# Kernel optimization log

Measured on AMD Instinct MI355X. Metric: run time of the kernel, lower is better.

## Reference

```python
import jax, jax.numpy as jnp
import numpy as np

B, L, C, H, FF = 2, 2048, 1024, 16, 4096
HD = C // H
SCALE = HD ** -0.5
EPS = 1e-5


def _ln(x, g, b):
    m = jnp.mean(x, axis=-1, keepdims=True)
    v = jnp.mean((x - m) ** 2, axis=-1, keepdims=True)
    return (x - m) * jax.lax.rsqrt(v + EPS) * g + b


def setup_inputs() -> dict:
    key = jax.random.key(0)
    ks = jax.random.split(key, 12)
    s = lambda fan_in: 1.0 / np.sqrt(fan_in)
    return {
        "x": jax.random.normal(ks[0], (B, L, C), jnp.float32),
        "freq_diff": jax.random.normal(ks[1], (B, L), jnp.float32),
        "qkv_w": jax.random.normal(ks[2], (C, 3 * C), jnp.float32) * s(C),
        "qkv_b": jnp.zeros((3 * C,), jnp.float32),
        "fp_w1": jax.random.normal(ks[3], (1, C), jnp.float32),
        "fp_b1": jnp.zeros((C,), jnp.float32),
        "fp_ln_g": jnp.ones((C,), jnp.float32),
        "fp_ln_b": jnp.zeros((C,), jnp.float32),
        "fp_w2": jax.random.normal(ks[4], (C, C), jnp.float32) * s(C),
        "fp_b2": jnp.zeros((C,), jnp.float32),
        "wq_w": jax.random.normal(ks[5], (HD, HD), jnp.float32) * s(HD),
        "wq_b": jnp.zeros((HD,), jnp.float32),
        "wk_w": jax.random.normal(ks[6], (HD, HD), jnp.float32) * s(HD),
        "wk_b": jnp.zeros((HD,), jnp.float32),
        "out_w": jax.random.normal(ks[7], (C, C), jnp.float32) * s(C),
        "out_b": jnp.zeros((C,), jnp.float32),
        "n1_g": jnp.ones((C,), jnp.float32),
        "n1_b": jnp.zeros((C,), jnp.float32),
        "n2_g": jnp.ones((C,), jnp.float32),
        "n2_b": jnp.zeros((C,), jnp.float32),
        "mlp_w1": jax.random.normal(ks[8], (C, FF), jnp.float32) * s(C),
        "mlp_b1": jnp.zeros((FF,), jnp.float32),
        "mlp_w2": jax.random.normal(ks[9], (FF, C), jnp.float32) * s(FF),
        "mlp_b2": jnp.zeros((C,), jnp.float32),
        "freq_scale": jnp.ones((1,), jnp.float32),
    }


def reference(x, freq_diff, qkv_w, qkv_b, fp_w1, fp_b1, fp_ln_g, fp_ln_b,
              fp_w2, fp_b2, wq_w, wq_b, wk_w, wk_b, out_w, out_b,
              n1_g, n1_b, n2_g, n2_b, mlp_w1, mlp_b1, mlp_w2, mlp_b2,
              freq_scale):
    shortcut = x
    xn = _ln(x, n1_g, n1_b)
    qkv = (xn @ qkv_w + qkv_b).reshape(B, L, 3, H, HD)
    qkv = jnp.transpose(qkv, (2, 0, 3, 1, 4))  # [3,B,H,L,HD]
    q, k, v = qkv[0], qkv[1], qkv[2]

    # frequency bias: MLP on scalar freq_diff -> per-head bias vectors
    fb = freq_diff[..., None] @ fp_w1 + fp_b1          # [B,L,C]
    fb = jax.nn.gelu(_ln(fb, fp_ln_g, fp_ln_b), approximate=False)
    fb = fb @ fp_w2 + fp_b2                            # [B,L,C]
    fb = jnp.transpose(fb.reshape(B, L, H, HD), (0, 2, 1, 3))  # [B,H,L,HD]
    qb = fb @ wq_w + wq_b
    kb = fb @ wk_w + wk_b
    freq_attn_bias = jnp.einsum('bhqd,bhkd->bhqk', qb, kb)

    attn = jnp.einsum('bhqd,bhkd->bhqk', q, k) * SCALE
    attn = attn + freq_scale[0] * freq_attn_bias
    attn = jax.nn.softmax(attn, axis=-1)
    o = jnp.einsum('bhqk,bhkd->bhqd', attn, v)
    o = jnp.transpose(o, (0, 2, 1, 3)).reshape(B, L, C)
    x = shortcut + (o @ out_w + out_b)

    xn2 = _ln(x, n2_g, n2_b)
    h = jax.nn.gelu(xn2 @ mlp_w1 + mlp_b1, approximate=False)
    x = x + (h @ mlp_w2 + mlp_b2)
    return x
```

## Files before the change

kernel.cpp:

```cpp
#include <hip/hip_runtime.h>
#include <math.h>


typedef __bf16 bf16;
typedef float f32x4 __attribute__((ext_vector_type(4)));
typedef bf16 bf16x8 __attribute__((ext_vector_type(8)));
typedef bf16 bf16x4 __attribute__((ext_vector_type(4)));

#define DEVINL __device__ __forceinline__

#define LOG2E 1.4426950408889634f

DEVINL float fast_exp2(float x) { return __builtin_amdgcn_exp2f(x); }

DEVINL void async_load16(const void* g, void* l) {
  __builtin_amdgcn_global_load_lds(
      (const __attribute__((address_space(1))) unsigned int*)g,
      (__attribute__((address_space(3))) unsigned int*)l, 16, 0, 0);
}

DEVINL f32x4 mfma16(bf16x8 a, bf16x8 b, f32x4 c) {
  return __builtin_amdgcn_mfma_f32_16x16x32_bf16(a, b, c, 0, 0, 0);
}

DEVINL float gelu_exact(float v) {
  return 0.5f * v * (1.0f + erff(v * 0.70710678118654752f));
}

DEVINL void hard_barrier() {
  asm volatile("" ::: "memory");
  __builtin_amdgcn_s_barrier();
  asm volatile("" ::: "memory");
}

DEVINL void block_reduce2(float& a, float& b, float* red, int tid) {
#pragma unroll
  for (int off = 32; off >= 1; off >>= 1) {
    a += __shfl_xor(a, off);
    b += __shfl_xor(b, off);
  }
  int w = tid >> 6;
  if ((tid & 63) == 0) { red[2 * w] = a; red[2 * w + 1] = b; }
  __syncthreads();
  a = red[0] + red[2] + red[4] + red[6];
  b = red[1] + red[3] + red[5] + red[7];
  __syncthreads();
}

__global__ __launch_bounds__(256) void pre_kernel(
    const float* __restrict__ qkv_w, const float* __restrict__ out_w,
    const float* __restrict__ mlp_w1, const float* __restrict__ mlp_w2,
    bf16* __restrict__ qkv_wt, bf16* __restrict__ out_wt,
    bf16* __restrict__ w1t, bf16* __restrict__ w2t,
    const float* __restrict__ x, const float* __restrict__ fd,
    const float* __restrict__ g1, const float* __restrict__ b1,
    const float* __restrict__ fw1, const float* __restrict__ fb1,
    const float* __restrict__ flg, const float* __restrict__ flb,
    bf16* __restrict__ xn, bf16* __restrict__ gout) {
  __shared__ float tile[32][33];
  __shared__ float red[8];
  const int id = blockIdx.x, t = threadIdx.x;
  if (id < 12288) {
    const float* W; bf16* Wt; int K, N, bx, by;
    if (id < 3072) {
      W = qkv_w; Wt = qkv_wt; K = 1024; N = 3072; bx = id % 96; by = id / 96;
    } else if (id < 4096) {
      int i = id - 3072;
      W = out_w; Wt = out_wt; K = 1024; N = 1024; bx = i & 31; by = i >> 5;
    } else if (id < 8192) {
      int i = id - 4096;
      W = mlp_w1; Wt = w1t; K = 1024; N = 4096; bx = i & 127; by = i >> 7;
    } else {
      int i = id - 8192;
      W = mlp_w2; Wt = w2t; K = 4096; N = 1024; bx = i & 31; by = i >> 5;
    }
    int n0 = bx * 32, k0 = by * 32;
    int tx = t & 31, ty = t >> 5;
#pragma unroll
    for (int r = 0; r < 4; ++r)
      tile[ty + r * 8][tx] = W[(size_t)(k0 + ty + r * 8) * N + n0 + tx];
    __syncthreads();
#pragma unroll
    for (int r = 0; r < 4; ++r)
      Wt[(size_t)(n0 + ty + r * 8) * K + k0 + tx] = (bf16)tile[tx][ty + r * 8];
    return;
  }
  int tok = id - 12288;
  float4 xv = ((const float4*)(x + (size_t)tok * 1024))[t];
  float s = xv.x + xv.y + xv.z + xv.w;
  float ss = xv.x * xv.x + xv.y * xv.y + xv.z * xv.z + xv.w * xv.w;
  block_reduce2(s, ss, red, t);
  float mean = s * (1.0f / 1024.0f);
  float rsig = rsqrtf(ss * (1.0f / 1024.0f) - mean * mean + 1e-5f);
  float4 g4 = ((const float4*)g1)[t], b4 = ((const float4*)b1)[t];
  bf16x4 o;
  o[0] = (bf16)((xv.x - mean) * rsig * g4.x + b4.x);
  o[1] = (bf16)((xv.y - mean) * rsig * g4.y + b4.y);
  o[2] = (bf16)((xv.z - mean) * rsig * g4.z + b4.z);
  o[3] = (bf16)((xv.w - mean) * rsig * g4.w + b4.w);
  ((bf16x4*)xn)[(size_t)tok * 256 + t] = o;

  float dv = fd[tok];
  float4 w4 = ((const float4*)fw1)[t], c4 = ((const float4*)fb1)[t];
  float f0 = dv * w4.x + c4.x, f1 = dv * w4.y + c4.y;
  float f2 = dv * w4.z + c4.z, f3 = dv * w4.w + c4.w;
  s = f0 + f1 + f2 + f3;
  ss = f0 * f0 + f1 * f1 + f2 * f2 + f3 * f3;
  block_reduce2(s, ss, red, t);
  mean = s * (1.0f / 1024.0f);
  rsig = rsqrtf(ss * (1.0f / 1024.0f) - mean * mean + 1e-5f);
  float4 lg = ((const float4*)flg)[t], lb = ((const float4*)flb)[t];
  bf16x4 q;
  q[0] = (bf16)gelu_exact((f0 - mean) * rsig * lg.x + lb.x);
  q[1] = (bf16)gelu_exact((f1 - mean) * rsig * lg.y + lb.y);
  q[2] = (bf16)gelu_exact((f2 - mean) * rsig * lg.z + lb.z);
  q[3] = (bf16)gelu_exact((f3 - mean) * rsig * lg.w + lb.w);
  ((bf16x4*)gout)[(size_t)tok * 256 + t] = q;
}

__global__ __launch_bounds__(256) void prec_qk(
    const float* __restrict__ fp_w2, const float* __restrict__ fp_b2,
    const float* __restrict__ wq_w, const float* __restrict__ wq_b,
    const float* __restrict__ wk_w, const float* __restrict__ wk_b,
    bf16* __restrict__ wqk2t, float* __restrict__ bqk) {
  __shared__ float Wl[64 * 64];
  __shared__ float Al[64 * 128];
  const int id = blockIdx.x;
  const int sel = id >> 7, h = (id >> 3) & 15, ck = id & 7;
  const int t = threadIdx.x;
  const float* wsel = sel ? wk_w : wq_w;
#pragma unroll
  for (int i = 0; i < 4; ++i)
    ((float4*)Wl)[i * 256 + t] = ((const float4*)wsel)[i * 256 + t];
  const int c0 = ck * 128, off = h * 64;
#pragma unroll
  for (int it = 0; it < 8; ++it) {
    int idx = it * 256 + t;
    int rr = idx >> 4, c4 = idx & 15;
    float4 v = *(const float4*)(fp_w2 + (size_t)(c0 + rr) * 1024 + off + c4 * 4);
    float vv[4] = {v.x, v.y, v.z, v.w};
#pragma unroll
    for (int k = 0; k < 4; ++k) {
      int i2 = c4 * 4 + k;
      Al[i2 * 128 + (rr ^ (i2 & 31))] = vv[k];
    }
  }
  __syncthreads();
  const int cr = t & 127, jh = (t >> 7) * 32;
  float acc[32];
#pragma unroll
  for (int j = 0; j < 32; ++j) acc[j] = 0.f;
  for (int i = 0; i < 64; ++i) {
    float a = Al[i * 128 + (cr ^ (i & 31))];
    const float4* wrow = (const float4*)(Wl + i * 64 + jh);
#pragma unroll
    for (int j4 = 0; j4 < 8; ++j4) {
      float4 wv = wrow[j4];
      acc[j4 * 4 + 0] += a * wv.x;
      acc[j4 * 4 + 1] += a * wv.y;
      acc[j4 * 4 + 2] += a * wv.z;
      acc[j4 * 4 + 3] += a * wv.w;
    }
  }
  const int nbase = sel * 1024 + off + jh;
#pragma unroll
  for (int j = 0; j < 32; ++j)
    wqk2t[(size_t)(nbase + j) * 1024 + c0 + cr] = (bf16)acc[j];
  if (ck == 0 && t < 64) {
    float s = 0.f;
    for (int i = 0; i < 64; ++i) s += fp_b2[off + i] * Wl[i * 64 + t];
    bqk[sel * 1024 + off + t] = s + (sel ? wk_b[t] : wq_b[t]);
  }
}

__global__ __launch_bounds__(256) void reduce_oln(
    const float* __restrict__ part, const float* __restrict__ x,
    const float* __restrict__ outb, const float* __restrict__ b2,
    const float* __restrict__ g, const float* __restrict__ bb,
    float* __restrict__ out0, bf16* __restrict__ ln2) {
  __shared__ float red[8];
  int tok = blockIdx.x, t = threadIdx.x;
  size_t base = (size_t)tok * 256 + t;
  const size_t S = (size_t)4096 * 256;
  float4 p0 = ((const float4*)part)[base];
  float4 p1 = ((const float4*)part)[base + S];
  float4 xv = ((const float4*)x)[base];
  float4 ob = ((const float4*)outb)[t];
  float v0 = xv.x + p0.x + p1.x + ob.x;
  float v1 = xv.y + p0.y + p1.y + ob.y;
  float v2 = xv.z + p0.z + p1.z + ob.z;
  float v3 = xv.w + p0.w + p1.w + ob.w;
  float s = v0 + v1 + v2 + v3;
  float ss = v0 * v0 + v1 * v1 + v2 * v2 + v3 * v3;
  block_reduce2(s, ss, red, t);
  float mean = s * (1.0f / 1024.0f);
  float rsig = rsqrtf(ss * (1.0f / 1024.0f) - mean * mean + 1e-5f);
  float4 g4 = ((const float4*)g)[t], bb4 = ((const float4*)bb)[t];
  bf16x4 o;
  o[0] = (bf16)((v0 - mean) * rsig * g4.x + bb4.x);
  o[1] = (bf16)((v1 - mean) * rsig * g4.y + bb4.y);
  o[2] = (bf16)((v2 - mean) * rsig * g4.z + bb4.z);
  o[3] = (bf16)((v3 - mean) * rsig * g4.w + bb4.w);
  ((bf16x4*)ln2)[base] = o;
  float4 b24 = ((const float4*)b2)[t];
  float4 ov;
  ov.x = v0 + b24.x; ov.y = v1 + b24.y; ov.z = v2 + b24.z; ov.w = v3 + b24.w;
  ((float4*)out0)[base] = ov;
}

#define PHASE(MH, NH, LA, LB, STAGE_STMT, WAIT_STMT)                          \
  do {                                                                        \
    if (LA) {                                                                 \
      _Pragma("unroll") for (int ml = 0; ml < 4; ++ml) {                      \
        _Pragma("unroll") for (int ks = 0; ks < 2; ++ks) {                    \
          const int rr = ml * 16 + lm;                                        \
          const int cc = (((ks * 4 + quad) ^ (lm & 7)) << 3);                 \
          af[ml][ks] = *(const bf16x8*)&As[bsel][MH][wm][rr][cc];             \
        }                                                                     \
      }                                                                       \
    }                                                                         \
    if (LB) {                                                                 \
      _Pragma("unroll") for (int nl = 0; nl < 2; ++nl) {                      \
        _Pragma("unroll") for (int ks = 0; ks < 2; ++ks) {                    \
          const int rr = nl * 16 + lm;                                        \
          const int cc = (((ks * 4 + quad) ^ (lm & 7)) << 3);                 \
          bfr[nl][ks] = *(const bf16x8*)&Bs[bsel][NH][wn][rr][cc];            \
        }                                                                     \
      }                                                                       \
    }                                                                         \
    STAGE_STMT;                                                               \
    WAIT_STMT;                                                                \
    hard_barrier();                                                           \
    __builtin_amdgcn_s_setprio(1);                                            \
    _Pragma("unroll") for (int ks = 0; ks < 2; ++ks) {                        \
      _Pragma("unroll") for (int ml = 0; ml < 4; ++ml) {                      \
        _Pragma("unroll") for (int nl = 0; nl < 2; ++nl) {                    \
          acc[(MH)*4 + ml][(NH)*2 + nl] = mfma16(                             \
              af[ml][ks], bfr[nl][ks], acc[(MH)*4 + ml][(NH)*2 + nl]);        \
        }                                                                     \
      }                                                                       \
    }                                                                         \
    __builtin_amdgcn_s_setprio(0);                                            \
  } while (0)

template <class Epi>
__global__ __launch_bounds__(512, 2) void gemm256(
    const bf16* __restrict__ A, const bf16* __restrict__ Bt,
    int lda, int ldb, int K, int kstride, int nbx, int nblk, int rowoffz,
    Epi epi) {
  __shared__ __align__(16) bf16 As[2][2][2][64][64];
  __shared__ __align__(16) bf16 Bs[2][2][4][32][64];

  const int tid = threadIdx.x;
  const int lane = tid & 63, w = tid >> 6;
  const int quad = lane >> 4, lm = lane & 15;
  const int wm = w >> 2, wn = w & 3;

  const int kz = blockIdx.x / nblk;
  const int bid = blockIdx.x - kz * nblk;
  const int swz = (nblk & 7) ? bid : ((bid & 7) * (nblk >> 3) + (bid >> 3));
  const int tm = swz / nbx, tn = swz - tm * nbx;
  const int m0 = tm << 8, n0 = tn << 8;
  const int rowoff = kz * rowoffz;
  A += (size_t)kz * kstride;
  Bt += (size_t)kz * kstride;

  const bf16* Abase = A + (size_t)m0 * lda;
  const bf16* Bbase = Bt + (size_t)n0 * ldb;

  auto stageA = [&](int b, int mh, int kt) {
#pragma unroll
    for (int j = 0; j < 2; ++j) {
      const int q = (w * 2 + j) * 64 + lane;
      const int wm2 = q >> 9, rr = (q >> 3) & 63, c = q & 7;
      async_load16(Abase + (size_t)(wm2 * 128 + mh * 64 + rr) * lda +
                       (size_t)kt * 64 + ((c ^ (rr & 7)) << 3),
                   (char*)&As[b][mh][0][0][0] + (w * 2 + j) * 1024);
    }
  };
  auto stageB = [&](int b, int nh, int kt) {
#pragma unroll
    for (int j = 0; j < 2; ++j) {
      const int q = (w * 2 + j) * 64 + lane;
      const int wn4 = q >> 8, rr = (q >> 3) & 31, c = q & 7;
      async_load16(Bbase + (size_t)(wn4 * 64 + nh * 32 + rr) * ldb +
                       (size_t)kt * 64 + ((c ^ (rr & 7)) << 3),
                   (char*)&Bs[b][nh][0][0][0] + (w * 2 + j) * 1024);
    }
  };

  f32x4 acc[8][4];
#pragma unroll
  for (int i = 0; i < 8; ++i)
#pragma unroll
    for (int j = 0; j < 4; ++j) {
      acc[i][j][0] = 0.f; acc[i][j][1] = 0.f;
      acc[i][j][2] = 0.f; acc[i][j][3] = 0.f;
    }
  bf16x8 af[4][2], bfr[2][2];

  stageA(0, 0, 0);
  stageB(0, 1, 0);
  stageA(0, 1, 0);
  stageB(0, 0, 0);
  stageA(1, 0, 1);
  stageB(1, 1, 1);
  asm volatile("s_waitcnt vmcnt(4)" ::: "memory");
  hard_barrier();

  const int nt = K >> 6;
  int bsel = 0;
  for (int t = 0; t < nt; ++t, bsel ^= 1) {
    PHASE(0, 0, 1, 1, { if (t + 1 < nt) stageA(bsel ^ 1, 1, t + 1); }, {});
    PHASE(0, 1, 0, 1, { if (t + 1 < nt) stageB(bsel ^ 1, 0, t + 1); }, {});
    PHASE(1, 1, 1, 0, { if (t + 2 < nt) stageA(bsel, 0, t + 2); }, {});
    PHASE(1, 0, 0, 1, { if (t + 2 < nt) stageB(bsel, 1, t + 2); },
          {
            if (t + 2 < nt) {
              asm volatile("s_waitcnt vmcnt(4)" ::: "memory");
            } else if (t + 1 < nt) {
              asm volatile("s_waitcnt vmcnt(0)" ::: "memory");
            }
          });
  }

#pragma unroll
  for (int mi = 0; mi < 8; ++mi)
#pragma unroll
    for (int ni = 0; ni < 4; ++ni)
      epi(rowoff + m0 + wm * 128 + mi * 16 + quad * 4,
          n0 + wn * 64 + ni * 16 + lm, acc[mi][ni]);
}

__global__ __launch_bounds__(256) void reduce_mlp2(
    const float* __restrict__ part, float* __restrict__ out) {
  size_t i = (size_t)blockIdx.x * 256 + threadIdx.x;
  const float4* p = (const float4*)part;
  float4 o = ((const float4*)out)[i];
  const size_t S = (size_t)4096 * 256;
  float4 a = p[i], b = p[i + S], c = p[i + 2 * S], d = p[i + 3 * S];
  o.x += a.x + b.x + c.x + d.x;
  o.y += a.y + b.y + c.y + d.y;
  o.z += a.z + b.z + c.z + d.z;
  o.w += a.w + b.w + c.w + d.w;
  ((float4*)out)[i] = o;
}

struct EpiQKV {
  const float* __restrict__ bias;
  bf16 *Qc, *Kc, *Vt;
  DEVINL void operator()(int row, int col, f32x4 v) const {
    int b = row >> 11, l = row & 2047;
    float bia = bias[col];
    if (col < 1024) {
      int h = col >> 6, d = col & 63;
      bf16* p = Qc + (size_t)(((b << 4) + h) * 2048 + l) * 128 + d;
#pragma unroll
      for (int r = 0; r < 4; ++r) p[r * 128] = (bf16)((v[r] + bia) * (0.125f * LOG2E));
    } else if (col < 2048) {
      int c2 = col - 1024, h = c2 >> 6, d = c2 & 63;
      bf16* p = Kc + (size_t)(((b << 4) + h) * 2048 + l) * 128 + d;
#pragma unroll
      for (int r = 0; r < 4; ++r) p[r * 128] = (bf16)(v[r] + bia);
    } else {
      int c2 = col - 2048, h = c2 >> 6, d = c2 & 63;
      bf16x4 pk;
#pragma unroll
      for (int r = 0; r < 4; ++r) pk[r] = (bf16)(v[r] + bia);
      *(bf16x4*)(Vt + (size_t)(((b << 4) + h) * 64 + d) * 2048 + l) = pk;
    }
  }
};

struct EpiQBKB {
  const float* __restrict__ bias;
  const float* __restrict__ fs;
  bf16 *Qc, *Kc;
  DEVINL void operator()(int row, int col, f32x4 v) const {
    int b = row >> 11, l = row & 2047;
    float bia = bias[col];
    if (col < 1024) {
      int h = col >> 6, d = col & 63;
      float sc = fs[0] * LOG2E;
      bf16* p = Qc + (size_t)(((b << 4) + h) * 2048 + l) * 128 + 64 + d;
#pragma unroll
      for (int r = 0; r < 4; ++r) p[r * 128] = (bf16)((v[r] + bia) * sc);
    } else {
      int c2 = col - 1024, h = c2 >> 6, d = c2 & 63;
      bf16* p = Kc + (size_t)(((b << 4) + h) * 2048 + l) * 128 + 64 + d;
#pragma unroll
      for (int r = 0; r < 4; ++r) p[r * 128] = (bf16)(v[r] + bia);
    }
  }
};

struct EpiMLP1 {
  const float* __restrict__ bias;
  bf16* hbf;
  DEVINL void operator()(int row, int col, f32x4 v) const {
    float bia = bias[col];
#pragma unroll
    for (int r = 0; r < 4; ++r)
      hbf[(size_t)(row + r) * 4096 + col] = (bf16)gelu_exact(v[r] + bia);
  }
};

struct EpiPart {
  float* part;
  DEVINL void operator()(int row, int col, f32x4 v) const {
#pragma unroll
    for (int r = 0; r < 4; ++r)
      part[(size_t)(row + r) * 1024 + col] = v[r];
  }
};

__global__ __launch_bounds__(512, 4) void flash_kernel(
    const bf16* __restrict__ Qc, const bf16* __restrict__ Kcp,
    const bf16* __restrict__ Vt, bf16* __restrict__ Obf) {
  __shared__ bf16 KsA[64 * 128];
  __shared__ bf16 KsB[64 * 128];
  __shared__ bf16 Ps[128 * 64];

  const int tid = threadIdx.x, lane = tid & 63, w = tid >> 6;
  const int quad = lane >> 4, lm = lane & 15;
  const int id = blockIdx.x;
  const int bh = id & 31, qt = id >> 5;
  const int b = bh >> 4, h = bh & 15;

  const bf16* Qg = Qc + ((size_t)bh * 2048 + qt * 128) * 128;
#pragma unroll
  for (int i = 0; i < 4; ++i) {
    int ch = i * 512 + tid, r = ch >> 4, cs = ch & 15, c = cs ^ (r & 7);
    char* dst = (i < 2) ? (char*)KsA + (i * 512 + w * 64) * 16
                        : (char*)KsB + ((i - 2) * 512 + w * 64) * 16;
    async_load16(Qg + (size_t)r * 128 + c * 8, dst);
  }
  __syncthreads();
  const int qr = w * 16 + lm;
  bf16x8 qf[4];
  {
    const bf16* base = (w < 4) ? KsA : KsB;
    int rr = qr & 63;
#pragma unroll
    for (int ks = 0; ks < 4; ++ks) {
      int pos = (ks * 4 + quad) ^ (lm & 7);
      qf[ks] = *(const bf16x8*)(base + rr * 128 + pos * 8);
    }
  }
  __syncthreads();

  float m_run = -3.0e38f, l_lane = 0.f;
  f32x4 o_acc[4];
#pragma unroll
  for (int nf = 0; nf < 4; ++nf) {
    o_acc[nf][0] = 0.f; o_acc[nf][1] = 0.f; o_acc[nf][2] = 0.f; o_acc[nf][3] = 0.f;
  }

  const bf16* Kg0 = Kcp + (size_t)bh * 2048 * 128;
  const bf16* Vg0 = Vt + (size_t)bh * 64 * 2048;

  auto stageK = [&](int kv, bf16* Kdst) {
    const bf16* Kg = Kg0 + (size_t)kv * 64 * 128;
#pragma unroll
    for (int i = 0; i < 2; ++i) {
      int ch = i * 512 + tid, key = ch >> 4, c = (ch & 15) ^ (key & 7);
      async_load16(Kg + (size_t)key * 128 + c * 8,
                   (char*)Kdst + (i * 512 + w * 64) * 16);
    }
  };

  stageK(0, KsA);

  for (int kv = 0; kv < 32; ++kv) {
    const bf16* Kcur = (kv & 1) ? KsB : KsA;
    __syncthreads();
    if (kv + 1 < 32) stageK(kv + 1, (kv & 1) ? KsA : KsB);

    bf16x8 vg[2][4];
    const bf16* Vg = Vg0 + kv * 64;
#pragma unroll
    for (int ks = 0; ks < 2; ++ks)
#pragma unroll
      for (int nf = 0; nf < 4; ++nf)
        vg[ks][nf] = *(const bf16x8*)(Vg + (size_t)(nf * 16 + lm) * 2048 +
                                      ks * 32 + quad * 8);

    f32x4 sa[4];
#pragma unroll
    for (int nk = 0; nk < 4; ++nk) {
      sa[nk][0] = 0.f; sa[nk][1] = 0.f; sa[nk][2] = 0.f; sa[nk][3] = 0.f;
    }
#pragma unroll
    for (int ks = 0; ks < 4; ++ks) {
      bf16x8 ak[4];
#pragma unroll
      for (int nk = 0; nk < 4; ++nk) {
        int key = nk * 16 + lm;
        int pos = (ks * 4 + quad) ^ (key & 7);
        ak[nk] = *(const bf16x8*)(Kcur + key * 128 + pos * 8);
      }
#pragma unroll
      for (int nk = 0; nk < 4; ++nk)
        sa[nk] = mfma16(ak[nk], qf[ks], sa[nk]);
    }

    float mx = fmaxf(fmaxf(sa[0][0], sa[0][1]), sa[0][2]);
    mx = fmaxf(fmaxf(mx, sa[0][3]), sa[1][0]);
    mx = fmaxf(fmaxf(mx, sa[1][1]), sa[1][2]);
    mx = fmaxf(fmaxf(mx, sa[1][3]), sa[2][0]);
    mx = fmaxf(fmaxf(mx, sa[2][1]), sa[2][2]);
    mx = fmaxf(fmaxf(mx, sa[2][3]), sa[3][0]);
    mx = fmaxf(fmaxf(mx, sa[3][1]), sa[3][2]);
    mx = fmaxf(mx, sa[3][3]);
    mx = fmaxf(mx, __shfl_xor(mx, 16));
    mx = fmaxf(mx, __shfl_xor(mx, 32));
    if (__any(mx > m_run + 8.0f)) {
      float mnew = fmaxf(m_run, mx);
      float alpha = fast_exp2(m_run - mnew);
      m_run = mnew;
      l_lane *= alpha;
#pragma unroll
      for (int nf = 0; nf < 4; ++nf) {
        o_acc[nf][0] *= alpha; o_acc[nf][1] *= alpha;
        o_acc[nf][2] *= alpha; o_acc[nf][3] *= alpha;
      }
    }
    float rs = 0.f;
#pragma unroll
    for (int nk = 0; nk < 4; ++nk)
#pragma unroll
      for (int rg = 0; rg < 4; ++rg) {
        float pv = fast_exp2(sa[nk][rg] - m_run);
        sa[nk][rg] = pv;
        rs += pv;
      }
    l_lane += rs;

#pragma unroll
    for (int nk = 0; nk < 4; ++nk) {
      int c16 = 2 * nk + (quad >> 1);
      int cs = c16 ^ (lm & 7);
      bf16x4 pk;
      pk[0] = (bf16)sa[nk][0]; pk[1] = (bf16)sa[nk][1];
      pk[2] = (bf16)sa[nk][2]; pk[3] = (bf16)sa[nk][3];
      *(bf16x4*)(Ps + qr * 64 + cs * 8 + (quad & 1) * 4) = pk;
    }

#pragma unroll
    for (int ks = 0; ks < 2; ++ks) {
      bf16x8 pa;
      {
        int cs = (ks * 4 + quad) ^ (lm & 7);
        pa = *(const bf16x8*)(Ps + qr * 64 + cs * 8);
      }
#pragma unroll
      for (int nf = 0; nf < 4; ++nf)
        o_acc[nf] = mfma16(vg[ks][nf], pa, o_acc[nf]);
    }
  }

  float lt = l_lane;
  lt += __shfl_xor(lt, 16);
  lt += __shfl_xor(lt, 32);
  float inv = 1.0f / lt;
  int l = qt * 128 + qr;
#pragma unroll
  for (int nf = 0; nf < 4; ++nf) {
    bf16x4 ov;
#pragma unroll
    for (int rg = 0; rg < 4; ++rg) ov[rg] = (bf16)(o_acc[nf][rg] * inv);
    int d = h * 64 + nf * 16 + quad * 4;
    *(bf16x4*)(Obf + ((size_t)b * 2048 + l) * 1024 + d) = ov;
  }
}

extern "C" void kernel_launch(void* const* d_in, const int* in_sizes, int n_in,
                              void* d_out, int out_size, void* d_ws, size_t ws_size,
                              hipStream_t stream) {
  (void)in_sizes; (void)n_in; (void)out_size; (void)ws_size;
  const float* x      = (const float*)d_in[0];
  const float* fd     = (const float*)d_in[1];
  const float* qkv_w  = (const float*)d_in[2];
  const float* qkv_b  = (const float*)d_in[3];
  const float* fp_w1  = (const float*)d_in[4];
  const float* fp_b1  = (const float*)d_in[5];
  const float* fp_ln_g= (const float*)d_in[6];
  const float* fp_ln_b= (const float*)d_in[7];
  const float* fp_w2  = (const float*)d_in[8];
  const float* fp_b2  = (const float*)d_in[9];
  const float* wq_w   = (const float*)d_in[10];
  const float* wq_b   = (const float*)d_in[11];
  const float* wk_w   = (const float*)d_in[12];
  const float* wk_b   = (const float*)d_in[13];
  const float* out_w  = (const float*)d_in[14];
  const float* out_b  = (const float*)d_in[15];
  const float* n1_g   = (const float*)d_in[16];
  const float* n1_b   = (const float*)d_in[17];
  const float* n2_g   = (const float*)d_in[18];
  const float* n2_b   = (const float*)d_in[19];
  const float* mlp_w1 = (const float*)d_in[20];
  const float* mlp_b1 = (const float*)d_in[21];
  const float* mlp_w2 = (const float*)d_in[22];
  const float* mlp_b2 = (const float*)d_in[23];
  const float* fscale = (const float*)d_in[24];
  float* out = (float*)d_out;

  char* p = (char*)d_ws;
  auto take = [&](size_t n) { char* r = p; p += (n + 255) & ~(size_t)255; return r; };
  bf16* xn_bf  = (bf16*)take((size_t)4096 * 1024 * 2);
  bf16* g_bf   = (bf16*)take((size_t)4096 * 1024 * 2);
  bf16* Qc     = (bf16*)take((size_t)32 * 2048 * 128 * 2);
  bf16* Kc     = (bf16*)take((size_t)32 * 2048 * 128 * 2);
  bf16* Vt     = (bf16*)take((size_t)32 * 64 * 2048 * 2);
  bf16* o_bf   = (bf16*)take((size_t)4096 * 1024 * 2);
  bf16* ln2_bf = (bf16*)take((size_t)4096 * 1024 * 2);
  bf16* h_bf   = (bf16*)take((size_t)4096 * 4096 * 2);
  bf16* qkv_wt = (bf16*)take((size_t)3072 * 1024 * 2);
  bf16* out_wt = (bf16*)take((size_t)1024 * 1024 * 2);
  bf16* w1t    = (bf16*)take((size_t)4096 * 1024 * 2);
  bf16* w2t    = (bf16*)take((size_t)1024 * 4096 * 2);
  bf16* wqk2t  = (bf16*)take((size_t)2048 * 1024 * 2);
  float* bqk   = (float*)take((size_t)2048 * 4);

  float* part = (float*)xn_bf;
  float* opart = (float*)h_bf;

  dim3 b256(256), b512(512);

  prec_qk<<<dim3(256), b256, 0, stream>>>(fp_w2, fp_b2, wq_w, wq_b, wk_w, wk_b, wqk2t, bqk);
  pre_kernel<<<dim3(16384), b256, 0, stream>>>(
      qkv_w, out_w, mlp_w1, mlp_w2, qkv_wt, out_wt, w1t, w2t,
      x, fd, n1_g, n1_b, fp_w1, fp_b1, fp_ln_g, fp_ln_b, xn_bf, g_bf);

  gemm256<<<dim3(192), b512, 0, stream>>>(xn_bf, qkv_wt, 1024, 1024, 1024, 0,
                                          12, 192, 0, EpiQKV{qkv_b, Qc, Kc, Vt});
  gemm256<<<dim3(128), b512, 0, stream>>>(g_bf, wqk2t, 1024, 1024, 1024, 0,
                                          8, 128, 0, EpiQBKB{bqk, fscale, Qc, Kc});
  flash_kernel<<<dim3(512), dim3(512), 0, stream>>>(Qc, Kc, Vt, o_bf);

  gemm256<<<dim3(128), b512, 0, stream>>>(o_bf, out_wt, 1024, 1024, 512, 512,
                                          4, 64, 4096, EpiPart{opart});
  reduce_oln<<<dim3(4096), b256, 0, stream>>>(opart, x, out_b, mlp_b2,
                                              n2_g, n2_b, out, ln2_bf);
  gemm256<<<dim3(256), b512, 0, stream>>>(ln2_bf, w1t, 1024, 1024, 1024, 0,
                                          16, 256, 0, EpiMLP1{mlp_b1, h_bf});
  gemm256<<<dim3(256), b512, 0, stream>>>(h_bf, w2t, 4096, 4096, 1024, 1024,
                                          4, 64, 4096, EpiPart{part});
  reduce_mlp2<<<dim3(4096), b256, 0, stream>>>(part, out);
}
```

Before: 517.7 us.

## Enlarge flash attention query tile to 256 rows and stage V through LDS

Each flash-attention block now processes 256 query rows (two 16-row groups per wave) instead of 128, which halves the grid and doubles reuse of each staged K tile. V tiles are now double-buffered into shared memory with async loads alongside K, rather than each wave reading them straight from global memory. Q fragments are loaded directly from global memory. The cost is more registers per thread (launch bounds lowered to 2 blocks), more LDS, and only 256 blocks, which may leave compute units underfilled.

```diff
diff --git a/kernel.cpp b/kernel.cpp
--- a/kernel.cpp
+++ b/kernel.cpp
@@ -414,52 +414,26 @@
   }
 };
 
-__global__ __launch_bounds__(512, 4) void flash_kernel(
+__global__ __launch_bounds__(512, 2) void flash_kernel(
     const bf16* __restrict__ Qc, const bf16* __restrict__ Kcp,
     const bf16* __restrict__ Vt, bf16* __restrict__ Obf) {
   __shared__ bf16 KsA[64 * 128];
   __shared__ bf16 KsB[64 * 128];
-  __shared__ bf16 Ps[128 * 64];
+  __shared__ bf16 VsA[64 * 64];
+  __shared__ bf16 VsB[64 * 64];
+  __shared__ bf16 Ps[256 * 64];
 
   const int tid = threadIdx.x, lane = tid & 63, w = tid >> 6;
   const int quad = lane >> 4, lm = lane & 15;
   const int id = blockIdx.x;
   const int bh = id & 31, qt = id >> 5;
   const int b = bh >> 4, h = bh & 15;
-
-  const bf16* Qg = Qc + ((size_t)bh * 2048 + qt * 128) * 128;
-#pragma unroll
-  for (int i = 0; i < 4; ++i) {
-    int ch = i * 512 + tid, r = ch >> 4, cs = ch & 15, c = cs ^ (r & 7);
-    char* dst = (i < 2) ? (char*)KsA + (i * 512 + w * 64) * 16
-                        : (char*)KsB + ((i - 2) * 512 + w * 64) * 16;
-    async_load16(Qg + (size_t)r * 128 + c * 8, dst);
-  }
-  __syncthreads();
-  const int qr = w * 16 + lm;
-  bf16x8 qf[4];
-  {
-    const bf16* base = (w < 4) ? KsA : KsB;
-    int rr = qr & 63;
-#pragma unroll
-    for (int ks = 0; ks < 4; ++ks) {
-      int pos = (ks * 4 + quad) ^ (lm & 7);
-      qf[ks] = *(const bf16x8*)(base + rr * 128 + pos * 8);
-    }
-  }
-  __syncthreads();
-
-  float m_run = -3.0e38f, l_lane = 0.f;
-  f32x4 o_acc[4];
-#pragma unroll
-  for (int nf = 0; nf < 4; ++nf) {
-    o_acc[nf][0] = 0.f; o_acc[nf][1] = 0.f; o_acc[nf][2] = 0.f; o_acc[nf][3] = 0.f;
-  }
+  const int qrw = w * 32;
 
   const bf16* Kg0 = Kcp + (size_t)bh * 2048 * 128;
   const bf16* Vg0 = Vt + (size_t)bh * 64 * 2048;
 
-  auto stageK = [&](int kv, bf16* Kdst) {
+  auto stage = [&](int kv, bf16* Kdst, bf16* Vdst) {
     const bf16* Kg = Kg0 + (size_t)kv * 64 * 128;
 #pragma unroll
     for (int i = 0; i < 2; ++i) {
@@ -467,29 +441,50 @@
       async_load16(Kg + (size_t)key * 128 + c * 8,
                    (char*)Kdst + (i * 512 + w * 64) * 16);
     }
+    {
+      int d = tid >> 3, c = (tid & 7) ^ (d & 7);
+      async_load16(Vg0 + (size_t)d * 2048 + kv * 64 + c * 8,
+                   (char*)Vdst + (w * 64) * 16);
+    }
   };
 
-  stageK(0, KsA);
+  stage(0, KsA, VsA);
+
+  const bf16* Qg = Qc + ((size_t)bh * 2048 + qt * 256) * 128;
+  bf16x8 qf[2][4];
+#pragma unroll
+  for (int qh = 0; qh < 2; ++qh)
+#pragma unroll
+    for (int ks = 0; ks < 4; ++ks)
+      qf[qh][ks] = *(const bf16x8*)(Qg + (size_t)(qrw + qh * 16 + lm) * 128 +
+                                    (ks * 4 + quad) * 8);
+
+  float m_run[2] = {-3.0e38f, -3.0e38f};
+  float l_lane[2] = {0.f, 0.f};
+  f32x4 o_acc[2][4];
+#pragma unroll
+  for (int qh = 0; qh < 2; ++qh)
+#pragma unroll
+    for (int nf = 0; nf < 4; ++nf) {
+      o_acc[qh][nf][0] = 0.f; o_acc[qh][nf][1] = 0.f;
+      o_acc[qh][nf][2] = 0.f; o_acc[qh][nf][3] = 0.f;
+    }
 
   for (int kv = 0; kv < 32; ++kv) {
     const bf16* Kcur = (kv & 1) ? KsB : KsA;
+    const bf16* Vcur = (kv & 1) ? VsB : VsA;
     __syncthreads();
-    if (kv + 1 < 32) stageK(kv + 1, (kv & 1) ? KsA : KsB);
-
-    bf16x8 vg[2][4];
-    const bf16* Vg = Vg0 + kv * 64;
-#pragma unroll
-    for (int ks = 0; ks < 2; ++ks)
-#pragma unroll
-      for (int nf = 0; nf < 4; ++nf)
-        vg[ks][nf] = *(const bf16x8*)(Vg + (size_t)(nf * 16 + lm) * 2048 +
-                                      ks * 32 + quad * 8);
-
-    f32x4 sa[4];
-#pragma unroll
-    for (int nk = 0; nk < 4; ++nk) {
-      sa[nk][0] = 0.f; sa[nk][1] = 0.f; sa[nk][2] = 0.f; sa[nk][3] = 0.f;
-    }
+    if (kv + 1 < 32)
+      stage(kv + 1, (kv & 1) ? KsA : KsB, (kv & 1) ? VsA : VsB);
+
+    f32x4 sa[2][4];
+#pragma unroll
+    for (int qh = 0; qh < 2; ++qh)
+#pragma unroll
+      for (int nk = 0; nk < 4; ++nk) {
+        sa[qh][nk][0] = 0.f; sa[qh][nk][1] = 0.f;
+        sa[qh][nk][2] = 0.f; sa[qh][nk][3] = 0.f;
+      }
 #pragma unroll
     for (int ks = 0; ks < 4; ++ks) {
       bf16x8 ak[4];
@@ -500,77 +495,96 @@
         ak[nk] = *(const bf16x8*)(Kcur + key * 128 + pos * 8);
       }
 #pragma unroll
+      for (int nk = 0; nk < 4; ++nk) {
+        sa[0][nk] = mfma16(ak[nk], qf[0][ks], sa[0][nk]);
+        sa[1][nk] = mfma16(ak[nk], qf[1][ks], sa[1][nk]);
+      }
+    }
+
+#pragma unroll
+    for (int qh = 0; qh < 2; ++qh) {
+      float mx = fmaxf(fmaxf(sa[qh][0][0], sa[qh][0][1]), sa[qh][0][2]);
+      mx = fmaxf(fmaxf(mx, sa[qh][0][3]), sa[qh][1][0]);
+      mx = fmaxf(fmaxf(mx, sa[qh][1][1]), sa[qh][1][2]);
+      mx = fmaxf(fmaxf(mx, sa[qh][1][3]), sa[qh][2][0]);
+      mx = fmaxf(fmaxf(mx, sa[qh][2][1]), sa[qh][2][2]);
+      mx = fmaxf(fmaxf(mx, sa[qh][2][3]), sa[qh][3][0]);
+      mx = fmaxf(fmaxf(mx, sa[qh][3][1]), sa[qh][3][2]);
+      mx = fmaxf(mx, sa[qh][3][3]);
+      mx = fmaxf(mx, __shfl_xor(mx, 16));
+      mx = fmaxf(mx, __shfl_xor(mx, 32));
+      if (__any(mx > m_run[qh] + 8.0f)) {
+        float mnew = fmaxf(m_run[qh], mx);
+        float alpha = fast_exp2(m_run[qh] - mnew);
+        m_run[qh] = mnew;
+        l_lane[qh] *= alpha;
+#pragma unroll
+        for (int nf = 0; nf < 4; ++nf) {
+          o_acc[qh][nf][0] *= alpha; o_acc[qh][nf][1] *= alpha;
+          o_acc[qh][nf][2] *= alpha; o_acc[qh][nf][3] *= alpha;
+        }
+      }
+      float rs = 0.f;
+#pragma unroll
       for (int nk = 0; nk < 4; ++nk)
-        sa[nk] = mfma16(ak[nk], qf[ks], sa[nk]);
-    }
-
-    float mx = fmaxf(fmaxf(sa[0][0], sa[0][1]), sa[0][2]);
-    mx = fmaxf(fmaxf(mx, sa[0][3]), sa[1][0]);
-    mx = fmaxf(fmaxf(mx, sa[1][1]), sa[1][2]);
-    mx = fmaxf(fmaxf(mx, sa[1][3]), sa[2][0]);
-    mx = fmaxf(fmaxf(mx, sa[2][1]), sa[2][2]);
-    mx = fmaxf(fmaxf(mx, sa[2][3]), sa[3][0]);
-    mx = fmaxf(fmaxf(mx, sa[3][1]), sa[3][2]);
-    mx = fmaxf(mx, sa[3][3]);
-    mx = fmaxf(mx, __shfl_xor(mx, 16));
-    mx = fmaxf(mx, __shfl_xor(mx, 32));
-    if (__any(mx > m_run + 8.0f)) {
-      float mnew = fmaxf(m_run, mx);
-      float alpha = fast_exp2(m_run - mnew);
-      m_run = mnew;
-      l_lane *= alpha;
+#pragma unroll
+        for (int rg = 0; rg < 4; ++rg) {
+          float pv = fast_exp2(sa[qh][nk][rg] - m_run[qh]);
+          sa[qh][nk][rg] = pv;
+          rs += pv;
+        }
+      l_lane[qh] += rs;
+
+      int qr = qrw + qh * 16 + lm;
+#pragma unroll
+      for (int nk = 0; nk < 4; ++nk) {
+        int c16 = 2 * nk + (quad >> 1);
+        int cs = c16 ^ (lm & 7);
+        bf16x4 pk;
+        pk[0] = (bf16)sa[qh][nk][0]; pk[1] = (bf16)sa[qh][nk][1];
+        pk[2] = (bf16)sa[qh][nk][2]; pk[3] = (bf16)sa[qh][nk][3];
+        *(bf16x4*)(Ps + qr * 64 + cs * 8 + (quad & 1) * 4) = pk;
+      }
+    }
+
+#pragma unroll
+    for (int ks = 0; ks < 2; ++ks) {
+      bf16x8 vb[4], pa[2];
 #pragma unroll
       for (int nf = 0; nf < 4; ++nf) {
-        o_acc[nf][0] *= alpha; o_acc[nf][1] *= alpha;
-        o_acc[nf][2] *= alpha; o_acc[nf][3] *= alpha;
+        int d = nf * 16 + lm;
+        int cs = (ks * 4 + quad) ^ (d & 7);
+        vb[nf] = *(const bf16x8*)(Vcur + d * 64 + cs * 8);
       }
-    }
-    float rs = 0.f;
-#pragma unroll
-    for (int nk = 0; nk < 4; ++nk)
-#pragma unroll
-      for (int rg = 0; rg < 4; ++rg) {
-        float pv = fast_exp2(sa[nk][rg] - m_run);
-        sa[nk][rg] = pv;
-        rs += pv;
+#pragma unroll
+      for (int qh = 0; qh < 2; ++qh) {
+        int qr = qrw + qh * 16 + lm;
+        int cs = (ks * 4 + quad) ^ (lm & 7);
+        pa[qh] = *(const bf16x8*)(Ps + qr * 64 + cs * 8);
       }
-    l_lane += rs;
-
-#pragma unroll
-    for (int nk = 0; nk < 4; ++nk) {
-      int c16 = 2 * nk + (quad >> 1);
-      int cs = c16 ^ (lm & 7);
-      bf16x4 pk;
-      pk[0] = (bf16)sa[nk][0]; pk[1] = (bf16)sa[nk][1];
-      pk[2] = (bf16)sa[nk][2]; pk[3] = (bf16)sa[nk][3];
-      *(bf16x4*)(Ps + qr * 64 + cs * 8 + (quad & 1) * 4) = pk;
-    }
-
-#pragma unroll
-    for (int ks = 0; ks < 2; ++ks) {
-      bf16x8 pa;
-      {
-        int cs = (ks * 4 + quad) ^ (lm & 7);
-        pa = *(const bf16x8*)(Ps + qr * 64 + cs * 8);
-      }
-#pragma unroll
-      for (int nf = 0; nf < 4; ++nf)
-        o_acc[nf] = mfma16(vg[ks][nf], pa, o_acc[nf]);
-    }
-  }
-
-  float lt = l_lane;
-  lt += __shfl_xor(lt, 16);
-  lt += __shfl_xor(lt, 32);
-  float inv = 1.0f / lt;
-  int l = qt * 128 + qr;
-#pragma unroll
-  for (int nf = 0; nf < 4; ++nf) {
-    bf16x4 ov;
-#pragma unroll
-    for (int rg = 0; rg < 4; ++rg) ov[rg] = (bf16)(o_acc[nf][rg] * inv);
-    int d = h * 64 + nf * 16 + quad * 4;
-    *(bf16x4*)(Obf + ((size_t)b * 2048 + l) * 1024 + d) = ov;
+#pragma unroll
+      for (int qh = 0; qh < 2; ++qh)
+#pragma unroll
+        for (int nf = 0; nf < 4; ++nf)
+          o_acc[qh][nf] = mfma16(vb[nf], pa[qh], o_acc[qh][nf]);
+    }
+  }
+
+#pragma unroll
+  for (int qh = 0; qh < 2; ++qh) {
+    float lt = l_lane[qh];
+    lt += __shfl_xor(lt, 16);
+    lt += __shfl_xor(lt, 32);
+    float inv = 1.0f / lt;
+    int l = qt * 256 + qrw + qh * 16 + lm;
+#pragma unroll
+    for (int nf = 0; nf < 4; ++nf) {
+      bf16x4 ov;
+#pragma unroll
+      for (int rg = 0; rg < 4; ++rg) ov[rg] = (bf16)(o_acc[qh][nf][rg] * inv);
+      int d = h * 64 + nf * 16 + quad * 4;
+      *(bf16x4*)(Obf + ((size_t)b * 2048 + l) * 1024 + d) = ov;
+    }
   }
 }
 
@@ -636,7 +650,7 @@
                                           12, 192, 0, EpiQKV{qkv_b, Qc, Kc, Vt});
   gemm256<<<dim3(128), b512, 0, stream>>>(g_bf, wqk2t, 1024, 1024, 1024, 0,
                                           8, 128, 0, EpiQBKB{bqk, fscale, Qc, Kc});
-  flash_kernel<<<dim3(512), dim3(512), 0, stream>>>(Qc, Kc, Vt, o_bf);
+  flash_kernel<<<dim3(256), dim3(512), 0, stream>>>(Qc, Kc, Vt, o_bf);
 
   gemm256<<<dim3(128), b512, 0, stream>>>(o_bf, out_wt, 1024, 1024, 512, 512,
                                           4, 64, 4096, EpiPart{opart});
```

New measurement: 446.1 us. 1.16x faster.
